# Kernel optimization log

Measured on AMD Instinct MI355X. Metric: run time of the kernel, lower is better.

## Reference

```python
import jax, jax.numpy as jnp
import numpy as np

B, S, H = 4096, 64, 256
NUM_STEPS = 200
DT = 0.01


def setup_inputs() -> dict:
    key = jax.random.key(0)
    ks = jax.random.split(key, 7)
    sc = lambda fan_in: 1.0 / np.sqrt(fan_in)
    return {
        "x0": jax.random.normal(ks[0], (B, S), dtype=jnp.float32),
        "W1": jax.random.normal(ks[1], (S, H), dtype=jnp.float32) * sc(S),
        "b1": jax.random.normal(ks[2], (H,), dtype=jnp.float32) * sc(S),
        "W2": jax.random.normal(ks[3], (H, H), dtype=jnp.float32) * sc(H),
        "b2": jax.random.normal(ks[4], (H,), dtype=jnp.float32) * sc(H),
        "W3": jax.random.normal(ks[5], (H, S), dtype=jnp.float32) * sc(H),
        "b3": jax.random.normal(ks[6], (S,), dtype=jnp.float32) * sc(H),
        "dt_scale": jnp.ones((1,), dtype=jnp.float32) * 0.01,
        "num_steps": NUM_STEPS,
    }


def reference(x0, W1, b1, W2, b2, W3, b3, dt_scale, num_steps):
    # Euler integration of dx/dt = MLP(x); trajectory = [x0, x1, ..., x_num_steps]
    def step(x, _):
        h = jnp.tanh(x @ W1 + b1)          # [B, H]
        h = jnp.tanh(h @ W2 + b2)          # [B, H]
        dx_dt = h @ W3 + b3                # [B, S]
        x_next = x + dx_dt * dt_scale * DT
        return x_next, x_next

    _, traj = jax.lax.scan(step, x0, None, length=num_steps)  # [T, B, S]
    traj = jnp.moveaxis(traj, 0, 1)                            # [B, T, S]
    return jnp.concatenate([x0[:, None, :], traj], axis=1)     # [B, T+1, S]
```

## Files before the change

kernel.cpp:

```cpp
#include <hip/hip_runtime.h>
#include <hip/hip_bf16.h>

typedef __bf16 bf16x8 __attribute__((ext_vector_type(8)));
typedef __bf16 bf16x4 __attribute__((ext_vector_type(4)));
typedef float  f32x4  __attribute__((ext_vector_type(4)));

__device__ __forceinline__ float fast_tanh(float x) {
    float e = __expf(2.0f * x);
    float r = __builtin_amdgcn_rcpf(e + 1.0f);
    return __builtin_fmaf(-2.0f, r, 1.0f);
}

__global__ void prep_weights(const float* __restrict__ W1,
                             const float* __restrict__ W2,
                             const float* __restrict__ W3,
                             __bf16* __restrict__ w1t,
                             __bf16* __restrict__ w2t,
                             __bf16* __restrict__ w3t) {
    int idx = blockIdx.x * blockDim.x + threadIdx.x;
    if (idx < 64 * 256) {
        int n = idx >> 6, k = idx & 63;
        w1t[idx] = (__bf16)W1[k * 256 + n];
    }
    int i2 = idx - 64 * 256;
    if (i2 >= 0 && i2 < 256 * 256) {
        int n = i2 >> 8, k = i2 & 255;
        w2t[i2] = (__bf16)W2[k * 256 + n];
    }
    int i3 = idx - 64 * 256 - 256 * 256;
    if (i3 >= 0 && i3 < 64 * 256) {
        int n = i3 >> 8, k = i3 & 255;
        w3t[i3] = (__bf16)W3[k * 64 + n];
    }
}

__global__ __launch_bounds__(512, 2)
void ode_kernel(const float* __restrict__ x0,
                const float* __restrict__ b1,
                const float* __restrict__ b2,
                const float* __restrict__ b3,
                const float* __restrict__ dt_scale,
                const int*   __restrict__ num_steps,
                const __bf16* __restrict__ w1t,
                const __bf16* __restrict__ w2t,
                const __bf16* __restrict__ w3t,
                float* __restrict__ out) {
    __shared__ float  xs[16][68];
    __shared__ __bf16 xb[16][72];
    __shared__ __align__(16) __bf16 h1[16 * 256];
    __shared__ __align__(16) __bf16 h2[16 * 256];

    const int tid  = threadIdx.x;
    const int wave = tid >> 6;
    const int lane = tid & 63;
    const int q    = lane >> 4;
    const int c    = lane & 15;
    const int cx8  = (c & 7) << 3;
    const int row0 = blockIdx.x * 16;

    const float scale = dt_scale[0] * 0.01f;
    const int   nT    = num_steps[0];

    bf16x8 w1f[2][2];
    #pragma unroll
    for (int kt = 0; kt < 2; ++kt)
        #pragma unroll
        for (int nt = 0; nt < 2; ++nt) {
            int n = wave * 32 + nt * 16 + c;
            w1f[kt][nt] = *(const bf16x8*)(w1t + n * 64 + kt * 32 + q * 8);
        }
    bf16x8 w2f[8][2];
    #pragma unroll
    for (int kt = 0; kt < 8; ++kt)
        #pragma unroll
        for (int nt = 0; nt < 2; ++nt) {
            int n = wave * 32 + nt * 16 + c;
            w2f[kt][nt] = *(const bf16x8*)(w2t + n * 256 + kt * 32 + q * 8);
        }
    bf16x8 w3f[8];
    f32x4  b3v4 = (f32x4){0.f, 0.f, 0.f, 0.f};
    if (wave < 4) {
        int n = wave * 16 + c;
        #pragma unroll
        for (int kt = 0; kt < 8; ++kt)
            w3f[kt] = *(const bf16x8*)(w3t + n * 256 + kt * 32 + q * 8);
        b3v4 = *(const f32x4*)(b3 + wave * 16 + q * 4);
    }
    f32x4 b1v4[2], b2v4[2];
    #pragma unroll
    for (int nt = 0; nt < 2; ++nt) {
        b1v4[nt] = *(const f32x4*)(b1 + wave * 32 + nt * 16 + q * 4);
        b2v4[nt] = *(const f32x4*)(b2 + wave * 32 + nt * 16 + q * 4);
    }

    const int mio = tid >> 5, sio = (tid & 31) * 2;
    float* outp = out + ((size_t)(row0 + mio) * 201) * 64 + sio;
    {
        const float2 v = *(const float2*)(x0 + (size_t)(row0 + mio) * 64 + sio);
        xs[mio][sio]     = v.x;  xs[mio][sio + 1] = v.y;
        xb[mio][sio]     = (__bf16)v.x;
        xb[mio][sio + 1] = (__bf16)v.y;
        *(float2*)outp = v;
        outp += 64;
    }
    __syncthreads();

    for (int t = 0; t < nT; ++t) {
        {
            f32x4 acc[2] = {b1v4[0], b1v4[1]};
            #pragma unroll
            for (int kt = 0; kt < 2; ++kt) {
                bf16x8 a = *(const bf16x8*)(&xb[c][kt * 32 + q * 8]);
                acc[0] = __builtin_amdgcn_mfma_f32_16x16x32_bf16(w1f[kt][0], a, acc[0], 0, 0, 0);
                acc[1] = __builtin_amdgcn_mfma_f32_16x16x32_bf16(w1f[kt][1], a, acc[1], 0, 0, 0);
            }
            #pragma unroll
            for (int nt = 0; nt < 2; ++nt) {
                bf16x4 o;
                #pragma unroll
                for (int r = 0; r < 4; ++r) o[r] = (__bf16)fast_tanh(acc[nt][r]);
                *(bf16x4*)(&h1[c * 256 + ((wave * 32 + nt * 16 + q * 4) ^ cx8)]) = o;
            }
        }
        __syncthreads();

        {
            f32x4 acc[2]  = {b2v4[0], b2v4[1]};
            f32x4 accB[2] = {(f32x4){0,0,0,0}, (f32x4){0,0,0,0}};
            #pragma unroll
            for (int kt = 0; kt < 4; ++kt) {
                bf16x8 a0 = *(const bf16x8*)(&h1[c * 256 + ((kt * 32 + q * 8) ^ cx8)]);
                bf16x8 a1 = *(const bf16x8*)(&h1[c * 256 + (((kt + 4) * 32 + q * 8) ^ cx8)]);
                acc[0]  = __builtin_amdgcn_mfma_f32_16x16x32_bf16(w2f[kt][0],     a0, acc[0],  0, 0, 0);
                acc[1]  = __builtin_amdgcn_mfma_f32_16x16x32_bf16(w2f[kt][1],     a0, acc[1],  0, 0, 0);
                accB[0] = __builtin_amdgcn_mfma_f32_16x16x32_bf16(w2f[kt + 4][0], a1, accB[0], 0, 0, 0);
                accB[1] = __builtin_amdgcn_mfma_f32_16x16x32_bf16(w2f[kt + 4][1], a1, accB[1], 0, 0, 0);
            }
            #pragma unroll
            for (int nt = 0; nt < 2; ++nt) {
                f32x4 s = acc[nt] + accB[nt];
                bf16x4 o;
                #pragma unroll
                for (int r = 0; r < 4; ++r) o[r] = (__bf16)fast_tanh(s[r]);
                *(bf16x4*)(&h2[c * 256 + ((wave * 32 + nt * 16 + q * 4) ^ cx8)]) = o;
            }
        }
        __syncthreads();

        if (wave < 4) {
            f32x4 acc  = b3v4;
            f32x4 accB = (f32x4){0, 0, 0, 0};
            #pragma unroll
            for (int kt = 0; kt < 4; ++kt) {
                bf16x8 a0 = *(const bf16x8*)(&h2[c * 256 + ((kt * 32 + q * 8) ^ cx8)]);
                bf16x8 a1 = *(const bf16x8*)(&h2[c * 256 + (((kt + 4) * 32 + q * 8) ^ cx8)]);
                acc  = __builtin_amdgcn_mfma_f32_16x16x32_bf16(w3f[kt],     a0, acc,  0, 0, 0);
                accB = __builtin_amdgcn_mfma_f32_16x16x32_bf16(w3f[kt + 4], a1, accB, 0, 0, 0);
            }
            acc += accB;
            f32x4 xv = *(f32x4*)(&xs[c][wave * 16 + q * 4]);
            xv += acc * scale;
            *(f32x4*)(&xs[c][wave * 16 + q * 4]) = xv;
            bf16x4 xbv;
            #pragma unroll
            for (int r = 0; r < 4; ++r) xbv[r] = (__bf16)xv[r];
            *(bf16x4*)(&xb[c][wave * 16 + q * 4]) = xbv;
        }
        __syncthreads();

        {
            float2 v = *(const float2*)(&xs[mio][sio]);
            *(float2*)outp = v;
            outp += 64;
        }
    }
}

extern "C" void kernel_launch(void* const* d_in, const int* in_sizes, int n_in,
                              void* d_out, int out_size, void* d_ws, size_t ws_size,
                              hipStream_t stream) {
    const float* x0 = (const float*)d_in[0];
    const float* W1 = (const float*)d_in[1];
    const float* b1 = (const float*)d_in[2];
    const float* W2 = (const float*)d_in[3];
    const float* b2 = (const float*)d_in[4];
    const float* W3 = (const float*)d_in[5];
    const float* b3 = (const float*)d_in[6];
    const float* dt = (const float*)d_in[7];
    const int*   ns = (const int*)d_in[8];

    __bf16* w1t = (__bf16*)d_ws;
    __bf16* w2t = w1t + 64 * 256;
    __bf16* w3t = w2t + 256 * 256;

    prep_weights<<<384, 256, 0, stream>>>(W1, W2, W3, w1t, w2t, w3t);

    int rows = in_sizes[0] / 64;
    ode_kernel<<<rows / 16, 512, 0, stream>>>(x0, b1, b2, b3, dt, ns,
                                              w1t, w2t, w3t, (float*)d_out);
}
```

Baseline: 443.4 us.

## Use 16 waves per block with one N-tile each; keep state in registers

New measurement: 464.3 us. 1.05x slower.

```diff
diff --git a/kernel.cpp b/kernel.cpp
--- a/kernel.cpp
+++ b/kernel.cpp
@@ -34,7 +34,7 @@
     }
 }
 
-__global__ __launch_bounds__(512, 2)
+__global__ __launch_bounds__(1024, 4)
 void ode_kernel(const float* __restrict__ x0,
                 const float* __restrict__ b1,
                 const float* __restrict__ b2,
@@ -45,7 +45,6 @@
                 const __bf16* __restrict__ w2t,
                 const __bf16* __restrict__ w3t,
                 float* __restrict__ out) {
-    __shared__ float  xs[16][68];
     __shared__ __bf16 xb[16][72];
     __shared__ __align__(16) __bf16 h1[16 * 256];
     __shared__ __align__(16) __bf16 h2[16 * 256];
@@ -61,94 +60,75 @@
     const float scale = dt_scale[0] * 0.01f;
     const int   nT    = num_steps[0];
 
-    bf16x8 w1f[2][2];
+    const int nw = wave * 16 + c;
+
+    bf16x8 w1f[2];
     #pragma unroll
     for (int kt = 0; kt < 2; ++kt)
-        #pragma unroll
-        for (int nt = 0; nt < 2; ++nt) {
-            int n = wave * 32 + nt * 16 + c;
-            w1f[kt][nt] = *(const bf16x8*)(w1t + n * 64 + kt * 32 + q * 8);
-        }
-    bf16x8 w2f[8][2];
+        w1f[kt] = *(const bf16x8*)(w1t + nw * 64 + kt * 32 + q * 8);
+    bf16x8 w2f[8];
     #pragma unroll
     for (int kt = 0; kt < 8; ++kt)
-        #pragma unroll
-        for (int nt = 0; nt < 2; ++nt) {
-            int n = wave * 32 + nt * 16 + c;
-            w2f[kt][nt] = *(const bf16x8*)(w2t + n * 256 + kt * 32 + q * 8);
-        }
+        w2f[kt] = *(const bf16x8*)(w2t + nw * 256 + kt * 32 + q * 8);
+
+    f32x4 b1v = *(const f32x4*)(b1 + wave * 16 + q * 4);
+    f32x4 b2v = *(const f32x4*)(b2 + wave * 16 + q * 4);
+
     bf16x8 w3f[8];
-    f32x4  b3v4 = (f32x4){0.f, 0.f, 0.f, 0.f};
+    f32x4  b3v = (f32x4){0.f, 0.f, 0.f, 0.f};
+    f32x4  xv  = (f32x4){0.f, 0.f, 0.f, 0.f};
+    float* outp = out;
     if (wave < 4) {
-        int n = wave * 16 + c;
         #pragma unroll
         for (int kt = 0; kt < 8; ++kt)
-            w3f[kt] = *(const bf16x8*)(w3t + n * 256 + kt * 32 + q * 8);
-        b3v4 = *(const f32x4*)(b3 + wave * 16 + q * 4);
-    }
-    f32x4 b1v4[2], b2v4[2];
-    #pragma unroll
-    for (int nt = 0; nt < 2; ++nt) {
-        b1v4[nt] = *(const f32x4*)(b1 + wave * 32 + nt * 16 + q * 4);
-        b2v4[nt] = *(const f32x4*)(b2 + wave * 32 + nt * 16 + q * 4);
-    }
-
-    const int mio = tid >> 5, sio = (tid & 31) * 2;
-    float* outp = out + ((size_t)(row0 + mio) * 201) * 64 + sio;
-    {
-        const float2 v = *(const float2*)(x0 + (size_t)(row0 + mio) * 64 + sio);
-        xs[mio][sio]     = v.x;  xs[mio][sio + 1] = v.y;
-        xb[mio][sio]     = (__bf16)v.x;
-        xb[mio][sio + 1] = (__bf16)v.y;
-        *(float2*)outp = v;
+            w3f[kt] = *(const bf16x8*)(w3t + nw * 256 + kt * 32 + q * 8);
+        b3v = *(const f32x4*)(b3 + wave * 16 + q * 4);
+        xv = *(const f32x4*)(x0 + (size_t)(row0 + c) * 64 + wave * 16 + q * 4);
+        outp = out + (size_t)(row0 + c) * 201 * 64 + wave * 16 + q * 4;
+        *(f32x4*)outp = xv;
         outp += 64;
+        bf16x4 xbv;
+        #pragma unroll
+        for (int r = 0; r < 4; ++r) xbv[r] = (__bf16)xv[r];
+        *(bf16x4*)(&xb[c][wave * 16 + q * 4]) = xbv;
     }
     __syncthreads();
 
     for (int t = 0; t < nT; ++t) {
         {
-            f32x4 acc[2] = {b1v4[0], b1v4[1]};
+            f32x4 acc = b1v;
             #pragma unroll
             for (int kt = 0; kt < 2; ++kt) {
                 bf16x8 a = *(const bf16x8*)(&xb[c][kt * 32 + q * 8]);
-                acc[0] = __builtin_amdgcn_mfma_f32_16x16x32_bf16(w1f[kt][0], a, acc[0], 0, 0, 0);
-                acc[1] = __builtin_amdgcn_mfma_f32_16x16x32_bf16(w1f[kt][1], a, acc[1], 0, 0, 0);
+                acc = __builtin_amdgcn_mfma_f32_16x16x32_bf16(w1f[kt], a, acc, 0, 0, 0);
             }
+            bf16x4 o;
             #pragma unroll
-            for (int nt = 0; nt < 2; ++nt) {
-                bf16x4 o;
-                #pragma unroll
-                for (int r = 0; r < 4; ++r) o[r] = (__bf16)fast_tanh(acc[nt][r]);
-                *(bf16x4*)(&h1[c * 256 + ((wave * 32 + nt * 16 + q * 4) ^ cx8)]) = o;
-            }
+            for (int r = 0; r < 4; ++r) o[r] = (__bf16)fast_tanh(acc[r]);
+            *(bf16x4*)(&h1[c * 256 + ((wave * 16 + q * 4) ^ cx8)]) = o;
         }
         __syncthreads();
 
         {
-            f32x4 acc[2]  = {b2v4[0], b2v4[1]};
-            f32x4 accB[2] = {(f32x4){0,0,0,0}, (f32x4){0,0,0,0}};
+            f32x4 acc  = b2v;
+            f32x4 accB = (f32x4){0, 0, 0, 0};
             #pragma unroll
             for (int kt = 0; kt < 4; ++kt) {
                 bf16x8 a0 = *(const bf16x8*)(&h1[c * 256 + ((kt * 32 + q * 8) ^ cx8)]);
                 bf16x8 a1 = *(const bf16x8*)(&h1[c * 256 + (((kt + 4) * 32 + q * 8) ^ cx8)]);
-                acc[0]  = __builtin_amdgcn_mfma_f32_16x16x32_bf16(w2f[kt][0],     a0, acc[0],  0, 0, 0);
-                acc[1]  = __builtin_amdgcn_mfma_f32_16x16x32_bf16(w2f[kt][1],     a0, acc[1],  0, 0, 0);
-                accB[0] = __builtin_amdgcn_mfma_f32_16x16x32_bf16(w2f[kt + 4][0], a1, accB[0], 0, 0, 0);
-                accB[1] = __builtin_amdgcn_mfma_f32_16x16x32_bf16(w2f[kt + 4][1], a1, accB[1], 0, 0, 0);
+                acc  = __builtin_amdgcn_mfma_f32_16x16x32_bf16(w2f[kt],     a0, acc,  0, 0, 0);
+                accB = __builtin_amdgcn_mfma_f32_16x16x32_bf16(w2f[kt + 4], a1, accB, 0, 0, 0);
             }
+            f32x4 s = acc + accB;
+            bf16x4 o;
             #pragma unroll
-            for (int nt = 0; nt < 2; ++nt) {
-                f32x4 s = acc[nt] + accB[nt];
-                bf16x4 o;
-                #pragma unroll
-                for (int r = 0; r < 4; ++r) o[r] = (__bf16)fast_tanh(s[r]);
-                *(bf16x4*)(&h2[c * 256 + ((wave * 32 + nt * 16 + q * 4) ^ cx8)]) = o;
-            }
+            for (int r = 0; r < 4; ++r) o[r] = (__bf16)fast_tanh(s[r]);
+            *(bf16x4*)(&h2[c * 256 + ((wave * 16 + q * 4) ^ cx8)]) = o;
         }
         __syncthreads();
 
         if (wave < 4) {
-            f32x4 acc  = b3v4;
+            f32x4 acc  = b3v;
             f32x4 accB = (f32x4){0, 0, 0, 0};
             #pragma unroll
             for (int kt = 0; kt < 4; ++kt) {
@@ -158,21 +138,15 @@
                 accB = __builtin_amdgcn_mfma_f32_16x16x32_bf16(w3f[kt + 4], a1, accB, 0, 0, 0);
             }
             acc += accB;
-            f32x4 xv = *(f32x4*)(&xs[c][wave * 16 + q * 4]);
             xv += acc * scale;
-            *(f32x4*)(&xs[c][wave * 16 + q * 4]) = xv;
             bf16x4 xbv;
             #pragma unroll
             for (int r = 0; r < 4; ++r) xbv[r] = (__bf16)xv[r];
             *(bf16x4*)(&xb[c][wave * 16 + q * 4]) = xbv;
+            *(f32x4*)outp = xv;
+            outp += 64;
         }
         __syncthreads();
-
-        {
-            float2 v = *(const float2*)(&xs[mio][sio]);
-            *(float2*)outp = v;
-            outp += 64;
-        }
     }
 }
 
@@ -196,6 +170,6 @@
     prep_weights<<<384, 256, 0, stream>>>(W1, W2, W3, w1t, w2t, w3t);
 
     int rows = in_sizes[0] / 64;
-    ode_kernel<<<rows / 16, 512, 0, stream>>>(x0, b1, b2, b3, dt, ns,
-                                              w1t, w2t, w3t, (float*)d_out);
+    ode_kernel<<<rows / 16, 1024, 0, stream>>>(x0, b1, b2, b3, dt, ns,
+                                               w1t, w2t, w3t, (float*)d_out);
 }
```
